# Kernel optimization log

Measured on AMD Instinct MI355X. Metric: run time of the kernel, lower is better.

## Reference

```python
import jax, jax.numpy as jnp
import numpy as np

N, E = 2048, 262144
SDIM, VDIM, EDIM = 256, 64, 32
NUM_ATOM_FEATURES, NUM_BOND_TYPES, NMOL = 16, 5, 64


def setup_inputs() -> dict:
    key = jax.random.key(0)
    ks = jax.random.split(key, 18)
    def lin(k, fan_in, shape):
        return jax.random.uniform(k, shape, jnp.float32, -1.0, 1.0) / np.sqrt(fan_in)
    inp = {
        "s": jax.random.normal(ks[0], (N, SDIM), jnp.float32),
        "v": jax.random.normal(ks[1], (N, 3, VDIM), jnp.float32),
        "p": jax.random.normal(ks[2], (N, 3), jnp.float32),
        "e": jax.random.normal(ks[3], (E, EDIM), jnp.float32),
        "batch": jnp.sort(jax.random.randint(ks[4], (N,), 0, NMOL)),
        "edge_index_global": jax.random.randint(ks[5], (2, E), 0, N),
        # learned params (torch DenseLayer == Linear): W [in,out], b [out]
        "Ws": lin(ks[6], SDIM, (SDIM, SDIM)),   "bs": lin(ks[7], SDIM, (SDIM,)),
        "Wc": lin(ks[8], VDIM, (VDIM, 1)),                                      # coords_lin, no bias
        "Wa": lin(ks[9], SDIM, (SDIM, NUM_ATOM_FEATURES)), "ba": lin(ks[10], SDIM, (NUM_ATOM_FEATURES,)),
        "Wb": lin(ks[11], EDIM, (EDIM, SDIM)),  "bb": lin(ks[12], EDIM, (SDIM,)),
        "W0": lin(ks[13], SDIM + 1, (SDIM + 1, SDIM)), "b0": lin(ks[14], SDIM + 1, (SDIM,)),
        "W1": lin(ks[15], SDIM, (SDIM, NUM_BOND_TYPES)), "b1": lin(ks[16], SDIM, (NUM_BOND_TYPES,)),
    }
    return inp


def reference(s, v, p, e, batch, edge_index_global,
              Ws, bs, Wc, Wa, ba, Wb, bb, W0, b0, W1, b1):
    # shared scalar mapping with SiLU
    s_h = jax.nn.silu(s @ Ws + bs)                              # [N, SDIM]
    coords = (v @ Wc)[..., 0]                                   # [N,3,VDIM]@[VDIM,1] -> [N,3]
    atoms_pred = s_h @ Wa + ba                                  # [N, NUM_ATOM_FEATURES]

    j, i = edge_index_global[0], edge_index_global[1]
    # coords_param == 'data': add positions then remove per-graph mean (scatter_mean)
    coords_pred = p + coords
    sums = jax.ops.segment_sum(coords_pred, batch, num_segments=NMOL)       # [NMOL,3]
    cnts = jax.ops.segment_sum(jnp.ones((N, 1), s.dtype), batch, num_segments=NMOL)
    coords_pred = coords_pred - (sums / jnp.maximum(cnts, 1.0))[batch]

    d = jnp.sum((coords_pred[i] - coords_pred[j]) ** 2, axis=-1, keepdims=True)  # [E,1]

    # dense edge matrix construction + symmetrization (as in the original)
    e_dense = jnp.zeros((N, N, EDIM), e.dtype).at[j, i].set(e)  # [N,N,EDIM]
    e_dense = 0.5 * (e_dense + jnp.swapaxes(e_dense, 0, 1))
    e_sym = e_dense[j, i]                                        # [E,EDIM]

    f = s_h[i] + s_h[j] + (e_sym @ Wb + bb)                      # [E,SDIM]
    edge = jnp.concatenate([f, d], axis=-1)                      # [E,SDIM+1]
    bonds_pred = jax.nn.silu(edge @ W0 + b0) @ W1 + b1           # [E,NUM_BOND_TYPES]
    return coords_pred, atoms_pred, bonds_pred
```

## Files before the change

### kernel.cpp

```cpp
#include <hip/hip_runtime.h>
#include <hip/hip_bf16.h>

typedef __bf16 bf16_8 __attribute__((ext_vector_type(8)));
typedef __bf16 bf16_4 __attribute__((ext_vector_type(4)));
typedef float f32x4 __attribute__((ext_vector_type(4)));

__device__ __forceinline__ float silu_f(float x) {
    return x * __builtin_amdgcn_rcpf(1.0f + __expf(-x));
}

__device__ __forceinline__ unsigned hslot(unsigned cell, unsigned nslots) {
    return (unsigned)(((unsigned long long)(cell * 2654435761u) * nslots) >> 32);
}
__device__ __forceinline__ int map_lookup(unsigned nslots, const int* __restrict__ M,
                                          const unsigned long long* __restrict__ H, unsigned cell) {
    if (nslots == 0) return M[cell] - 1;
    unsigned slot = hslot(cell, nslots);
    for (int pr = 0; pr < 4096; pr++) {
        unsigned long long v = H[slot];
        if (v == 0ull) return -1;
        if ((unsigned)(v >> 32) == cell) return (int)(v & 0xFFFFFFFFu) - 1;
        slot++; if (slot == nslots) slot = 0;
    }
    return -1;
}

__global__ __launch_bounds__(256) void kS(float* __restrict__ out, int n, float val) {
    int i = blockIdx.x * 256 + threadIdx.x;
    if (i < n) out[i] = val;
}

__global__ __launch_bounds__(256, 4) void kP(
    const float* __restrict__ s, const float* __restrict__ Ws, const float* __restrict__ bs,
    const float* __restrict__ W0, const float* __restrict__ Wa, const float* __restrict__ ba,
    const float* __restrict__ v, const float* __restrict__ p,
    const float* __restrict__ Wc, const float* __restrict__ Wb, const float* __restrict__ bb,
    const float* __restrict__ b0, const float* __restrict__ W1,
    const int* __restrict__ batch, const int* __restrict__ ei,
    int N, int E, int gaB, int coordB, int mapB,
    unsigned nslots, int* __restrict__ M, unsigned long long* __restrict__ H,
    __bf16* __restrict__ G, __bf16* __restrict__ wqT, __bf16* __restrict__ w1Tg,
    float* __restrict__ w0L, float* __restrict__ b0p,
    float* __restrict__ cp, float* __restrict__ sums, float* __restrict__ cnts,
    float* __restrict__ outA)
{
    __shared__ __align__(16) char LDSC[37376];
    int b = blockIdx.x, t = threadIdx.x;

    if (b < gaB) {
        __bf16* s_bf  = (__bf16*)LDSC;
        __bf16* sh_bf = (__bf16*)(LDSC + 8448);
        __bf16* wT    = (__bf16*)(LDSC + 16896);
        int wv = t >> 6, lane = t & 63;
        int l16 = lane & 15, q8 = (lane >> 4) * 8, r4b = (lane >> 4) * 4;
        int r0 = b * 16;
        {
            int row = t >> 4, c0 = (t & 15) * 16;
            const float* sp = s + (long long)(r0 + row) * 256 + c0;
            bool ok = (r0 + row) < N;
            f32x4 a0 = ok ? *(const f32x4*)(sp + 0)  : (f32x4){0.f,0.f,0.f,0.f};
            f32x4 a1 = ok ? *(const f32x4*)(sp + 4)  : (f32x4){0.f,0.f,0.f,0.f};
            f32x4 a2 = ok ? *(const f32x4*)(sp + 8)  : (f32x4){0.f,0.f,0.f,0.f};
            f32x4 a3 = ok ? *(const f32x4*)(sp + 12) : (f32x4){0.f,0.f,0.f,0.f};
            bf16_8 p0, p1;
#pragma unroll
            for (int q = 0; q < 4; q++) {
                p0[q] = (__bf16)a0[q]; p0[q + 4] = (__bf16)a1[q];
                p1[q] = (__bf16)a2[q]; p1[q + 4] = (__bf16)a3[q];
            }
            *(bf16_8*)(s_bf + row * 264 + c0) = p0;
            *(bf16_8*)(s_bf + row * 264 + c0 + 8) = p1;
        }
        __syncthreads();
        __bf16* wTw = wT + wv * 2560;
        float ld[32];

        f32x4 acc[4];
#pragma unroll
        for (int ct = 0; ct < 4; ct++) acc[ct] = (f32x4){0.f,0.f,0.f,0.f};
        {
            const float* wp = Ws + wv * 64 + lane;
#pragma unroll
            for (int i = 0; i < 32; i++) ld[i] = wp[i * 256];
#pragma unroll 1
            for (int kk = 0; kk < 8; kk++) {
#pragma unroll
                for (int j = 0; j < 4; j++) {
                    bf16_8 pk;
#pragma unroll
                    for (int q = 0; q < 8; q++) pk[q] = (__bf16)ld[j * 8 + q];
                    *(bf16_8*)(wTw + lane * 40 + j * 8) = pk;
                }
                if (kk < 7) {
                    const float* wpn = wp + (kk + 1) * 32 * 256;
#pragma unroll
                    for (int i = 0; i < 32; i++) ld[i] = wpn[i * 256];
                }
                bf16_8 af = *(const bf16_8*)(s_bf + l16 * 264 + kk * 32 + q8);
#pragma unroll
                for (int ct = 0; ct < 4; ct++) {
                    bf16_8 bfr = *(const bf16_8*)(wTw + (ct * 16 + l16) * 40 + q8);
                    acc[ct] = __builtin_amdgcn_mfma_f32_16x16x32_bf16(af, bfr, acc[ct], 0, 0, 0);
                }
            }
        }
#pragma unroll
        for (int ct = 0; ct < 4; ct++) {
            int col = wv * 64 + ct * 16 + l16;
            float bsv = bs[col];
#pragma unroll
            for (int r = 0; r < 4; r++)
                sh_bf[(r4b + r) * 264 + col] = (__bf16)silu_f(acc[ct][r] + bsv);
        }
        __syncthreads();

        if (wv == 0) {
            f32x4 aa = (f32x4){0.f,0.f,0.f,0.f};
#pragma unroll 1
            for (int ks = 0; ks < 8; ks++) {
                bf16_8 a = *(const bf16_8*)(sh_bf + l16 * 264 + ks * 32 + q8);
                bf16_8 wb;
#pragma unroll
                for (int j = 0; j < 8; j++) wb[j] = (__bf16)Wa[(ks * 32 + q8 + j) * 16 + l16];
                aa = __builtin_amdgcn_mfma_f32_16x16x32_bf16(a, wb, aa, 0, 0, 0);
            }
            float bav = ba[l16];
#pragma unroll
            for (int r = 0; r < 4; r++) {
                int row = r0 + r4b + r;
                if (row < N) outA[row * 16 + l16] = aa[r] + bav;
            }
        }

        f32x4 acc2[4];
#pragma unroll
        for (int ct = 0; ct < 4; ct++) acc2[ct] = (f32x4){0.f,0.f,0.f,0.f};
        {
            const float* wp = W0 + wv * 64 + lane;
#pragma unroll
            for (int i = 0; i < 32; i++) ld[i] = wp[i * 256];
#pragma unroll 1
            for (int kk = 0; kk < 8; kk++) {
#pragma unroll
                for (int j = 0; j < 4; j++) {
                    bf16_8 pk;
#pragma unroll
                    for (int q = 0; q < 8; q++) pk[q] = (__bf16)ld[j * 8 + q];
                    *(bf16_8*)(wTw + lane * 40 + j * 8) = pk;
                }
                if (kk < 7) {
                    const float* wpn = wp + (kk + 1) * 32 * 256;
#pragma unroll
                    for (int i = 0; i < 32; i++) ld[i] = wpn[i * 256];
                }
                bf16_8 af = *(const bf16_8*)(sh_bf + l16 * 264 + kk * 32 + q8);
#pragma unroll
                for (int ct = 0; ct < 4; ct++) {
                    bf16_8 bfr = *(const bf16_8*)(wTw + (ct * 16 + l16) * 40 + q8);
                    acc2[ct] = __builtin_amdgcn_mfma_f32_16x16x32_bf16(af, bfr, acc2[ct], 0, 0, 0);
                }
            }
        }
#pragma unroll
        for (int ct = 0; ct < 4; ct++) {
            int col = wv * 64 + ct * 16 + l16;
#pragma unroll
            for (int r = 0; r < 4; r++) {
                int row = r0 + r4b + r;
                if (row < N) G[(long long)row * 256 + col] = (__bf16)acc2[ct][r];
            }
        }
        return;
    }
    b -= gaB;

    float* sm = (float*)LDSC;
    if (b < 2) {
        int r0 = b * 16;
        for (int i4 = t; i4 < 1024; i4 += 256)
            ((f32x4*)sm)[i4] = ((const f32x4*)(Wb + r0 * 256))[i4];
        __syncthreads();
        float acc[16];
#pragma unroll
        for (int r = 0; r < 16; r++) acc[r] = 0.f;
        for (int m4 = 0; m4 < 64; m4++) {
            float w0v = W0[(m4 * 4 + 0) * 256 + t];
            float w1v = W0[(m4 * 4 + 1) * 256 + t];
            float w2v = W0[(m4 * 4 + 2) * 256 + t];
            float w3v = W0[(m4 * 4 + 3) * 256 + t];
#pragma unroll
            for (int r = 0; r < 16; r++) {
                f32x4 sv = *(const f32x4*)(sm + r * 256 + m4 * 4);
                acc[r] += sv[0] * w0v + sv[1] * w1v + sv[2] * w2v + sv[3] * w3v;
            }
        }
#pragma unroll
        for (int r = 0; r < 16; r++) wqT[t * 32 + r0 + r] = (__bf16)acc[r];
        return;
    }
    b -= 2;
    if (b < 1) {
        sm[t] = bb[t];
        __syncthreads();
        float acc = 0.f;
        for (int m4 = 0; m4 < 64; m4++) {
            f32x4 bv = *(const f32x4*)(sm + m4 * 4);
            acc += bv[0] * W0[(m4 * 4 + 0) * 256 + t] + bv[1] * W0[(m4 * 4 + 1) * 256 + t]
                 + bv[2] * W0[(m4 * 4 + 2) * 256 + t] + bv[3] * W0[(m4 * 4 + 3) * 256 + t];
        }
        b0p[t] = acc + b0[t];
        w0L[t] = W0[256 * 256 + t];
#pragma unroll
        for (int c = 0; c < 16; c++)
            w1Tg[c * 256 + t] = (c < 5) ? (__bf16)W1[t * 5 + c] : (__bf16)0.f;
        return;
    }
    b -= 1;
    if (b < coordB) {
        int n = b * 256 + t;
        if (t < 64) sm[t] = Wc[t];
        __syncthreads();
        if (n < N) {
            int mb = batch[n] & 1023;
#pragma unroll
            for (int ax = 0; ax < 3; ax++) {
                float acc = 0.f;
                for (int d4 = 0; d4 < 16; d4++) {
                    f32x4 vv = *(const f32x4*)(v + (long long)n * 192 + ax * 64 + d4 * 4);
                    f32x4 wv2 = *(const f32x4*)(sm + d4 * 4);
                    acc += vv[0] * wv2[0] + vv[1] * wv2[1] + vv[2] * wv2[2] + vv[3] * wv2[3];
                }
                float val = p[n * 3 + ax] + acc;
                cp[n * 3 + ax] = val;
                atomicAdd(&sums[mb * 3 + ax], val);
            }
            atomicAdd(&cnts[mb], 1.0f);
        }
        return;
    }
    b -= coordB;
    {
        int k = b * 256 + t;
        if (k < E) {
            int jj = ei[k], ii = ei[E + k];
            if ((unsigned)jj >= (unsigned)N) jj = 0;
            if ((unsigned)ii >= (unsigned)N) ii = 0;
            unsigned cell = (unsigned)jj * (unsigned)N + (unsigned)ii;
            if (nslots == 0) {
                atomicMax(&M[cell], k + 1);
            } else {
                unsigned long long mine = ((unsigned long long)cell << 32) | (unsigned)(k + 1);
                unsigned slot = hslot(cell, nslots);
                for (int pr = 0; pr < 4096; pr++) {
                    unsigned long long old = atomicCAS(&H[slot], 0ull, mine);
                    if (old == 0ull) break;
                    if ((unsigned)(old >> 32) == cell) { atomicMax(&H[slot], mine); break; }
                    slot++; if (slot == nslots) slot = 0;
                }
            }
        }
    }
}

__global__ __launch_bounds__(256, 4) void kC(
    const float* __restrict__ e, const int* __restrict__ ei, const int* __restrict__ batch,
    int N, int E, int edgeB, unsigned nslots,
    const int* __restrict__ M, const unsigned long long* __restrict__ H,
    const __bf16* __restrict__ G, const __bf16* __restrict__ wqTg,
    const __bf16* __restrict__ w1Tg,
    const float* __restrict__ w0L, const float* __restrict__ b0p,
    const float* __restrict__ cp, const float* __restrict__ sums, const float* __restrict__ cnts,
    const float* __restrict__ b1,
    float* __restrict__ outC, float* __restrict__ bonds)
{
    if (blockIdx.x >= (unsigned)edgeB) {
        int n = ((int)blockIdx.x - edgeB) * 256 + threadIdx.x;
        if (n < N) {
            int mb = batch[n] & 1023;
            float cnt = fmaxf(cnts[mb], 1.0f);
#pragma unroll
            for (int ax = 0; ax < 3; ax++)
                outC[n * 3 + ax] = cp[n * 3 + ax] - sums[mb * 3 + ax] / cnt;
        }
        return;
    }

    __shared__ __align__(16) __bf16 esym[64 * 40];
    __shared__ __align__(16) __bf16 hbuf[64 * 264];
    __shared__ float sd[64];
    __shared__ int si[64], sj[64], sm1[64], sm2[64];

    int t = threadIdx.x;
    int wv = t >> 6, lane = t & 63;
    int l16 = lane & 15, q8 = (lane >> 4) * 8;
    int e0 = blockIdx.x * 64;

    if (t < 128) {
        int tt = t & 63;
        int k = e0 + tt;
        if (t < 64) {
            if (k >= E) {
                si[tt] = 0; sj[tt] = 0; sm1[tt] = 0; sd[tt] = 0.f;
            } else {
                int jj = ei[k], ii = ei[E + k];
                if ((unsigned)jj >= (unsigned)N) jj = 0;
                if ((unsigned)ii >= (unsigned)N) ii = 0;
                si[tt] = ii; sj[tt] = jj;
                int m1 = map_lookup(nslots, M, H, (unsigned)jj * (unsigned)N + (unsigned)ii);
                sm1[tt] = ((unsigned)m1 < (unsigned)E) ? m1 : 0;
                int bi = batch[ii] & 1023, bj = batch[jj] & 1023;
                float inv_i = __builtin_amdgcn_rcpf(fmaxf(cnts[bi], 1.0f));
                float inv_j = __builtin_amdgcn_rcpf(fmaxf(cnts[bj], 1.0f));
                float dx = (cp[ii * 3 + 0] - sums[bi * 3 + 0] * inv_i) - (cp[jj * 3 + 0] - sums[bj * 3 + 0] * inv_j);
                float dy = (cp[ii * 3 + 1] - sums[bi * 3 + 1] * inv_i) - (cp[jj * 3 + 1] - sums[bj * 3 + 1] * inv_j);
                float dz = (cp[ii * 3 + 2] - sums[bi * 3 + 2] * inv_i) - (cp[jj * 3 + 2] - sums[bj * 3 + 2] * inv_j);
                sd[tt] = dx * dx + dy * dy + dz * dz;
            }
        } else {
            if (k >= E) {
                sm2[tt] = -1;
            } else {
                int jj = ei[k], ii = ei[E + k];
                if ((unsigned)jj >= (unsigned)N) jj = 0;
                if ((unsigned)ii >= (unsigned)N) ii = 0;
                int m2 = map_lookup(nslots, M, H, (unsigned)ii * (unsigned)N + (unsigned)jj);
                sm2[tt] = ((unsigned)m2 < (unsigned)E) ? m2 : -1;
            }
        }
    }
    __syncthreads();

    {
        int er = t >> 2, qg = (t & 3) * 8;
        int m1 = sm1[er], m2 = sm2[er];
        const float* e1p = e + (size_t)m1 * 32 + qg;
        float v1[8], v2[8];
#pragma unroll
        for (int q = 0; q < 8; q++) { v1[q] = e1p[q]; v2[q] = 0.f; }
        if (m2 >= 0) {
            const float* e2p = e + (size_t)m2 * 32 + qg;
#pragma unroll
            for (int q = 0; q < 8; q++) v2[q] = e2p[q];
        }
        bf16_8 es;
#pragma unroll
        for (int q = 0; q < 8; q++) es[q] = (__bf16)(0.5f * (v1[q] + v2[q]));
        *(bf16_8*)(esym + er * 40 + qg) = es;
    }
    {
        int c4 = lane * 4;
        for (int it = 0; it < 16; it++) {
            int er = wv * 16 + it;
            bf16_4 gi = *(const bf16_4*)(G + (size_t)si[er] * 256 + c4);
            bf16_4 gj = *(const bf16_4*)(G + (size_t)sj[er] * 256 + c4);
            bf16_4 o;
#pragma unroll
            for (int q = 0; q < 4; q++) o[q] = (__bf16)((float)gi[q] + (float)gj[q]);
            *(bf16_4*)(hbuf + er * 264 + c4) = o;
        }
    }
    __syncthreads();

    f32x4 acc[4][4];
#pragma unroll
    for (int rt = 0; rt < 4; rt++)
#pragma unroll
        for (int ct = 0; ct < 4; ct++)
            acc[rt][ct] = (f32x4){0.f, 0.f, 0.f, 0.f};
    bf16_8 af[4];
#pragma unroll
    for (int rt = 0; rt < 4; rt++)
        af[rt] = *(const bf16_8*)(esym + (rt * 16 + l16) * 40 + q8);
#pragma unroll
    for (int ct = 0; ct < 4; ct++) {
        int c = (wv * 4 + ct) * 16 + l16;
        bf16_8 bfr = *(const bf16_8*)(wqTg + c * 32 + q8);
#pragma unroll
        for (int rt = 0; rt < 4; rt++)
            acc[rt][ct] = __builtin_amdgcn_mfma_f32_16x16x32_bf16(af[rt], bfr, acc[rt][ct], 0, 0, 0);
    }
    int r4base = (lane >> 4) * 4;
    f32x4 sdv[4];
#pragma unroll
    for (int rt = 0; rt < 4; rt++)
        sdv[rt] = *(const f32x4*)(sd + rt * 16 + r4base);
#pragma unroll
    for (int ct = 0; ct < 4; ct++) {
        int col = (wv * 4 + ct) * 16 + l16;
        float w0c = w0L[col], b0c = b0p[col];
#pragma unroll
        for (int rt = 0; rt < 4; rt++) {
#pragma unroll
            for (int r4 = 0; r4 < 4; r4++) {
                int row = rt * 16 + r4base + r4;
                int off = row * 264 + col;
                float x = acc[rt][ct][r4] + b0c + sdv[rt][r4] * w0c + (float)hbuf[off];
                hbuf[off] = (__bf16)silu_f(x);
            }
        }
    }
    __syncthreads();

    f32x4 acc3 = {0.f, 0.f, 0.f, 0.f};
#pragma unroll
    for (int ks = 0; ks < 8; ks++) {
        bf16_8 a = *(const bf16_8*)(hbuf + (wv * 16 + l16) * 264 + ks * 32 + q8);
        bf16_8 b2 = *(const bf16_8*)(w1Tg + l16 * 256 + ks * 32 + q8);
        acc3 = __builtin_amdgcn_mfma_f32_16x16x32_bf16(a, b2, acc3, 0, 0, 0);
    }
    if (l16 < 5) {
        float bv = b1[l16];
#pragma unroll
        for (int r4 = 0; r4 < 4; r4++) {
            int row = wv * 16 + r4base + r4;
            if (e0 + row < E)
                bonds[(size_t)(e0 + row) * 5 + l16] = acc3[r4] + bv;
        }
    }
}

extern "C" void kernel_launch(void* const* d_in, const int* in_sizes, int n_in,
                              void* d_out, int out_size, void* d_ws, size_t ws_size,
                              hipStream_t stream)
{
    const float* s  = (const float*)d_in[0];
    const float* v  = (const float*)d_in[1];
    const float* p  = (const float*)d_in[2];
    const float* e  = (const float*)d_in[3];
    const int* batch = (const int*)d_in[4];
    const int* ei    = (const int*)d_in[5];
    const float* Ws = (const float*)d_in[6];
    const float* bs = (const float*)d_in[7];
    const float* Wc = (const float*)d_in[8];
    const float* Wa = (const float*)d_in[9];
    const float* ba = (const float*)d_in[10];
    const float* Wb = (const float*)d_in[11];
    const float* bb = (const float*)d_in[12];
    const float* W0 = (const float*)d_in[13];
    const float* b0 = (const float*)d_in[14];
    const float* W1 = (const float*)d_in[15];
    const float* b1 = (const float*)d_in[16];

    float* out = (float*)d_out;
    int sentN = out_size < 8192 ? out_size : 8192;

    int N = in_sizes[0] / 256;
    long long E = in_sizes[5] / 2;
    int code = 0;
    if (in_sizes[6] != 65536) code |= 1;
    if (in_sizes[8] != 64) code |= 2;
    if (in_sizes[11] != 32 * 256) code |= 4;
    if (in_sizes[9] != 16 * 256) code |= 8;
    if (in_sizes[15] != 5 * 256) code |= 16;
    if (in_sizes[13] != 257 * 256) code |= 32;
    if (N < 1 || in_sizes[0] != N * 256) code |= 64;
    if (in_sizes[1] != (long long)N * 192) code |= 128;
    if (in_sizes[2] != N * 3) code |= 256;
    if (in_sizes[3] != E * 32) code |= 512;
    if (in_sizes[4] != N) code |= 1024;
    if ((long long)out_size != 19LL * N + 5LL * E) code |= 2048;
    if (code) {
        kS<<<(sentN + 255) / 256, 256, 0, stream>>>(out, sentN, 3000.0f + 64.0f * (float)code);
        return;
    }
    int Ei = (int)E;

    auto align256 = [](size_t x) { return (x + 255) & ~(size_t)255; };
    size_t G_b  = align256((size_t)N * 512);
    size_t cp_b = align256((size_t)N * 12);
    size_t misc = G_b + 16384 + 8192 + 1024 + 1024 + cp_b + 12288 + 4096 + 256;
    size_t denseB = (size_t)N * (size_t)N * 4;
    unsigned nslots; size_t mapBytes;
    if (ws_size >= denseB + misc) {
        nslots = 0; mapBytes = denseB;
    } else {
        size_t avail = (ws_size > misc) ? (ws_size - misc) / 8 : 0;
        size_t want = (size_t)Ei * 2;
        size_t ns = avail < want ? avail : want;
        if (ns < (size_t)Ei + (size_t)Ei / 8) {
            unsigned mb = (unsigned)(ws_size >> 20); if (mb > 120) mb = 120;
            kS<<<(sentN + 255) / 256, 256, 0, stream>>>(out, sentN, 1000.0f + 8.0f * (float)mb);
            return;
        }
        nslots = (unsigned)ns; mapBytes = ns * 8;
    }

    char* ws = (char*)d_ws;
    int* M = (int*)ws;
    unsigned long long* H = (unsigned long long*)ws;
    size_t off = align256(mapBytes);
    __bf16* G    = (__bf16*)(ws + off); off += G_b;
    __bf16* wqT  = (__bf16*)(ws + off); off += 16384;
    __bf16* w1Tg = (__bf16*)(ws + off); off += 8192;
    float* w0L  = (float*)(ws + off);  off += 1024;
    float* b0p  = (float*)(ws + off);  off += 1024;
    float* cp   = (float*)(ws + off);  off += cp_b;
    float* sums = (float*)(ws + off);  off += 12288;
    float* cnts = (float*)(ws + off);  off += 4096;

    float* outC = out;
    float* outA = outC + 3 * N;
    float* outB = outC + 19 * N;

    (void)hipMemsetAsync(ws, 0x00, mapBytes, stream);
    (void)hipMemsetAsync(sums, 0x00, 12288 + 4096, stream);

    int mapB = (Ei + 255) / 256;
    int coordB = (N + 255) / 256;
    int gaB = (N + 15) / 16;
    kP<<<gaB + 3 + coordB + mapB, 256, 0, stream>>>(
        s, Ws, bs, W0, Wa, ba, v, p, Wc, Wb, bb, b0, W1, batch, ei,
        N, Ei, gaB, coordB, mapB, nslots, M, H,
        G, wqT, w1Tg, w0L, b0p, cp, sums, cnts, outA);
    int edgeB = (Ei + 63) / 64;
    kC<<<edgeB + coordB, 256, 0, stream>>>(
        e, ei, batch, N, Ei, edgeB, nslots, M, H, G, wqT, w1Tg,
        w0L, b0p, cp, sums, cnts, b1, outC, outB);
}
```

Before: 196.1 us.

## Split weight prep into separate kernel, pre-transpose weights, restructure edge MLP

Weight conversion to transposed bf16 (Ws, W0, Wa) moves into a new prep kernel kW. The node GEMM kernel kP is split four ways across column quarters and reads the pre-transposed weights directly from global memory instead of restaging them through LDS. The two hipMemsetAsync calls are replaced by one custom zero kernel. In the edge kernel, the G gather and the bias/SiLU epilogue are fused into registers per edge, so the hbuf staging pass and one block barrier are removed. In exchange there is one more kernel launch and the first node-level GEMM is recomputed four times per row block.

```diff
diff --git a/kernel.cpp b/kernel.cpp
--- a/kernel.cpp
+++ b/kernel.cpp
@@ -30,151 +30,30 @@
     if (i < n) out[i] = val;
 }
 
-__global__ __launch_bounds__(256, 4) void kP(
-    const float* __restrict__ s, const float* __restrict__ Ws, const float* __restrict__ bs,
-    const float* __restrict__ W0, const float* __restrict__ Wa, const float* __restrict__ ba,
+__global__ __launch_bounds__(256) void kZ(f32x4* __restrict__ a, size_t na16,
+                                          f32x4* __restrict__ b, size_t nb16) {
+    size_t i = (size_t)blockIdx.x * 256 + threadIdx.x;
+    size_t stride = (size_t)gridDim.x * 256;
+    f32x4 z = {0.f, 0.f, 0.f, 0.f};
+    for (size_t k = i; k < na16; k += stride) a[k] = z;
+    for (size_t k = i; k < nb16; k += stride) b[k] = z;
+}
+
+__global__ __launch_bounds__(256) void kW(
     const float* __restrict__ v, const float* __restrict__ p,
-    const float* __restrict__ Wc, const float* __restrict__ Wb, const float* __restrict__ bb,
-    const float* __restrict__ b0, const float* __restrict__ W1,
     const int* __restrict__ batch, const int* __restrict__ ei,
-    int N, int E, int gaB, int coordB, int mapB,
+    const float* __restrict__ Wc, const float* __restrict__ Ws, const float* __restrict__ Wa,
+    const float* __restrict__ Wb, const float* __restrict__ bb,
+    const float* __restrict__ W0, const float* __restrict__ b0, const float* __restrict__ W1,
+    int N, int E, int coordB, int mapB,
     unsigned nslots, int* __restrict__ M, unsigned long long* __restrict__ H,
-    __bf16* __restrict__ G, __bf16* __restrict__ wqT, __bf16* __restrict__ w1Tg,
+    __bf16* __restrict__ wqT, __bf16* __restrict__ w1Tg,
+    __bf16* __restrict__ WsT, __bf16* __restrict__ W0T, __bf16* __restrict__ WaT,
     float* __restrict__ w0L, float* __restrict__ b0p,
-    float* __restrict__ cp, float* __restrict__ sums, float* __restrict__ cnts,
-    float* __restrict__ outA)
+    float* __restrict__ cp, float* __restrict__ sums, float* __restrict__ cnts)
 {
-    __shared__ __align__(16) char LDSC[37376];
+    __shared__ float sm[16 * 256];
     int b = blockIdx.x, t = threadIdx.x;
-
-    if (b < gaB) {
-        __bf16* s_bf  = (__bf16*)LDSC;
-        __bf16* sh_bf = (__bf16*)(LDSC + 8448);
-        __bf16* wT    = (__bf16*)(LDSC + 16896);
-        int wv = t >> 6, lane = t & 63;
-        int l16 = lane & 15, q8 = (lane >> 4) * 8, r4b = (lane >> 4) * 4;
-        int r0 = b * 16;
-        {
-            int row = t >> 4, c0 = (t & 15) * 16;
-            const float* sp = s + (long long)(r0 + row) * 256 + c0;
-            bool ok = (r0 + row) < N;
-            f32x4 a0 = ok ? *(const f32x4*)(sp + 0)  : (f32x4){0.f,0.f,0.f,0.f};
-            f32x4 a1 = ok ? *(const f32x4*)(sp + 4)  : (f32x4){0.f,0.f,0.f,0.f};
-            f32x4 a2 = ok ? *(const f32x4*)(sp + 8)  : (f32x4){0.f,0.f,0.f,0.f};
-            f32x4 a3 = ok ? *(const f32x4*)(sp + 12) : (f32x4){0.f,0.f,0.f,0.f};
-            bf16_8 p0, p1;
-#pragma unroll
-            for (int q = 0; q < 4; q++) {
-                p0[q] = (__bf16)a0[q]; p0[q + 4] = (__bf16)a1[q];
-                p1[q] = (__bf16)a2[q]; p1[q + 4] = (__bf16)a3[q];
-            }
-            *(bf16_8*)(s_bf + row * 264 + c0) = p0;
-            *(bf16_8*)(s_bf + row * 264 + c0 + 8) = p1;
-        }
-        __syncthreads();
-        __bf16* wTw = wT + wv * 2560;
-        float ld[32];
-
-        f32x4 acc[4];
-#pragma unroll
-        for (int ct = 0; ct < 4; ct++) acc[ct] = (f32x4){0.f,0.f,0.f,0.f};
-        {
-            const float* wp = Ws + wv * 64 + lane;
-#pragma unroll
-            for (int i = 0; i < 32; i++) ld[i] = wp[i * 256];
-#pragma unroll 1
-            for (int kk = 0; kk < 8; kk++) {
-#pragma unroll
-                for (int j = 0; j < 4; j++) {
-                    bf16_8 pk;
-#pragma unroll
-                    for (int q = 0; q < 8; q++) pk[q] = (__bf16)ld[j * 8 + q];
-                    *(bf16_8*)(wTw + lane * 40 + j * 8) = pk;
-                }
-                if (kk < 7) {
-                    const float* wpn = wp + (kk + 1) * 32 * 256;
-#pragma unroll
-                    for (int i = 0; i < 32; i++) ld[i] = wpn[i * 256];
-                }
-                bf16_8 af = *(const bf16_8*)(s_bf + l16 * 264 + kk * 32 + q8);
-#pragma unroll
-                for (int ct = 0; ct < 4; ct++) {
-                    bf16_8 bfr = *(const bf16_8*)(wTw + (ct * 16 + l16) * 40 + q8);
-                    acc[ct] = __builtin_amdgcn_mfma_f32_16x16x32_bf16(af, bfr, acc[ct], 0, 0, 0);
-                }
-            }
-        }
-#pragma unroll
-        for (int ct = 0; ct < 4; ct++) {
-            int col = wv * 64 + ct * 16 + l16;
-            float bsv = bs[col];
-#pragma unroll
-            for (int r = 0; r < 4; r++)
-                sh_bf[(r4b + r) * 264 + col] = (__bf16)silu_f(acc[ct][r] + bsv);
-        }
-        __syncthreads();
-
-        if (wv == 0) {
-            f32x4 aa = (f32x4){0.f,0.f,0.f,0.f};
-#pragma unroll 1
-            for (int ks = 0; ks < 8; ks++) {
-                bf16_8 a = *(const bf16_8*)(sh_bf + l16 * 264 + ks * 32 + q8);
-                bf16_8 wb;
-#pragma unroll
-                for (int j = 0; j < 8; j++) wb[j] = (__bf16)Wa[(ks * 32 + q8 + j) * 16 + l16];
-                aa = __builtin_amdgcn_mfma_f32_16x16x32_bf16(a, wb, aa, 0, 0, 0);
-            }
-            float bav = ba[l16];
-#pragma unroll
-            for (int r = 0; r < 4; r++) {
-                int row = r0 + r4b + r;
-                if (row < N) outA[row * 16 + l16] = aa[r] + bav;
-            }
-        }
-
-        f32x4 acc2[4];
-#pragma unroll
-        for (int ct = 0; ct < 4; ct++) acc2[ct] = (f32x4){0.f,0.f,0.f,0.f};
-        {
-            const float* wp = W0 + wv * 64 + lane;
-#pragma unroll
-            for (int i = 0; i < 32; i++) ld[i] = wp[i * 256];
-#pragma unroll 1
-            for (int kk = 0; kk < 8; kk++) {
-#pragma unroll
-                for (int j = 0; j < 4; j++) {
-                    bf16_8 pk;
-#pragma unroll
-                    for (int q = 0; q < 8; q++) pk[q] = (__bf16)ld[j * 8 + q];
-                    *(bf16_8*)(wTw + lane * 40 + j * 8) = pk;
-                }
-                if (kk < 7) {
-                    const float* wpn = wp + (kk + 1) * 32 * 256;
-#pragma unroll
-                    for (int i = 0; i < 32; i++) ld[i] = wpn[i * 256];
-                }
-                bf16_8 af = *(const bf16_8*)(sh_bf + l16 * 264 + kk * 32 + q8);
-#pragma unroll
-                for (int ct = 0; ct < 4; ct++) {
-                    bf16_8 bfr = *(const bf16_8*)(wTw + (ct * 16 + l16) * 40 + q8);
-                    acc2[ct] = __builtin_amdgcn_mfma_f32_16x16x32_bf16(af, bfr, acc2[ct], 0, 0, 0);
-                }
-            }
-        }
-#pragma unroll
-        for (int ct = 0; ct < 4; ct++) {
-            int col = wv * 64 + ct * 16 + l16;
-#pragma unroll
-            for (int r = 0; r < 4; r++) {
-                int row = r0 + r4b + r;
-                if (row < N) G[(long long)row * 256 + col] = (__bf16)acc2[ct][r];
-            }
-        }
-        return;
-    }
-    b -= gaB;
-
-    float* sm = (float*)LDSC;
     if (b < 2) {
         int r0 = b * 16;
         for (int i4 = t; i4 < 1024; i4 += 256)
@@ -213,6 +92,30 @@
 #pragma unroll
         for (int c = 0; c < 16; c++)
             w1Tg[c * 256 + t] = (c < 5) ? (__bf16)W1[t * 5 + c] : (__bf16)0.f;
+        return;
+    }
+    b -= 1;
+    if (b < 4) {
+        for (int idx = t; idx < 64 * 256; idx += 256) {
+            int kl = idx >> 8, c = idx & 255;
+            WsT[c * 256 + b * 64 + kl] = (__bf16)Ws[(b * 64 + kl) * 256 + c];
+        }
+        return;
+    }
+    b -= 4;
+    if (b < 4) {
+        for (int idx = t; idx < 64 * 256; idx += 256) {
+            int kl = idx >> 8, c = idx & 255;
+            W0T[c * 256 + b * 64 + kl] = (__bf16)W0[(b * 64 + kl) * 256 + c];
+        }
+        return;
+    }
+    b -= 4;
+    if (b < 1) {
+        for (int idx = t; idx < 4096; idx += 256) {
+            int k = idx >> 4, c = idx & 15;
+            WaT[c * 256 + k] = (__bf16)Wa[k * 16 + c];
+        }
         return;
     }
     b -= 1;
@@ -262,6 +165,91 @@
     }
 }
 
+__global__ __launch_bounds__(256, 4) void kP(
+    const float* __restrict__ s, const float* __restrict__ bs, const float* __restrict__ ba,
+    const __bf16* __restrict__ WsT, const __bf16* __restrict__ W0T, const __bf16* __restrict__ WaT,
+    int N, __bf16* __restrict__ G, float* __restrict__ outA)
+{
+    __shared__ __align__(16) __bf16 s_bf[16 * 264];
+    __shared__ __align__(16) __bf16 sh_bf[16 * 264];
+    int b = blockIdx.x, t = threadIdx.x;
+    int rb = b >> 2, cq = b & 3;
+    int r0 = rb * 16;
+    int wv = t >> 6, lane = t & 63;
+    int l16 = lane & 15, q = lane >> 4, q8 = q * 8;
+
+    {
+        int row = t >> 4, c0 = (t & 15) * 16;
+        const float* sp = s + (long long)(r0 + row) * 256 + c0;
+        bool ok = (r0 + row) < N;
+        f32x4 a0 = ok ? *(const f32x4*)(sp + 0)  : (f32x4){0.f,0.f,0.f,0.f};
+        f32x4 a1 = ok ? *(const f32x4*)(sp + 4)  : (f32x4){0.f,0.f,0.f,0.f};
+        f32x4 a2 = ok ? *(const f32x4*)(sp + 8)  : (f32x4){0.f,0.f,0.f,0.f};
+        f32x4 a3 = ok ? *(const f32x4*)(sp + 12) : (f32x4){0.f,0.f,0.f,0.f};
+        bf16_8 p0, p1;
+#pragma unroll
+        for (int qq = 0; qq < 4; qq++) {
+            p0[qq] = (__bf16)a0[qq]; p0[qq + 4] = (__bf16)a1[qq];
+            p1[qq] = (__bf16)a2[qq]; p1[qq + 4] = (__bf16)a3[qq];
+        }
+        *(bf16_8*)(s_bf + row * 264 + c0) = p0;
+        *(bf16_8*)(s_bf + row * 264 + c0 + 8) = p1;
+    }
+    __syncthreads();
+
+    f32x4 acc[4];
+#pragma unroll
+    for (int ct = 0; ct < 4; ct++) acc[ct] = (f32x4){0.f,0.f,0.f,0.f};
+#pragma unroll
+    for (int kk = 0; kk < 8; kk++) {
+        bf16_8 af = *(const bf16_8*)(s_bf + l16 * 264 + kk * 32 + q8);
+#pragma unroll
+        for (int ct = 0; ct < 4; ct++) {
+            bf16_8 bw = *(const bf16_8*)(WsT + (size_t)(wv * 64 + ct * 16 + l16) * 256 + kk * 32 + q8);
+            acc[ct] = __builtin_amdgcn_mfma_f32_16x16x32_bf16(af, bw, acc[ct], 0, 0, 0);
+        }
+    }
+#pragma unroll
+    for (int ct = 0; ct < 4; ct++) {
+        int col = wv * 64 + ct * 16 + l16;
+        float bsv = bs[col];
+#pragma unroll
+        for (int r = 0; r < 4; r++)
+            sh_bf[(q * 4 + r) * 264 + col] = (__bf16)silu_f(acc[ct][r] + bsv);
+    }
+    __syncthreads();
+
+    f32x4 a2c = (f32x4){0.f,0.f,0.f,0.f};
+    int gcol = cq * 64 + wv * 16 + l16;
+#pragma unroll
+    for (int kk = 0; kk < 8; kk++) {
+        bf16_8 af = *(const bf16_8*)(sh_bf + l16 * 264 + kk * 32 + q8);
+        bf16_8 bw = *(const bf16_8*)(W0T + (size_t)gcol * 256 + kk * 32 + q8);
+        a2c = __builtin_amdgcn_mfma_f32_16x16x32_bf16(af, bw, a2c, 0, 0, 0);
+    }
+#pragma unroll
+    for (int r = 0; r < 4; r++) {
+        int row = r0 + q * 4 + r;
+        if (row < N) G[(long long)row * 256 + gcol] = (__bf16)a2c[r];
+    }
+
+    if (cq == 0 && wv == 0) {
+        f32x4 aa = (f32x4){0.f,0.f,0.f,0.f};
+#pragma unroll
+        for (int ks = 0; ks < 8; ks++) {
+            bf16_8 af = *(const bf16_8*)(sh_bf + l16 * 264 + ks * 32 + q8);
+            bf16_8 bw = *(const bf16_8*)(WaT + (size_t)l16 * 256 + ks * 32 + q8);
+            aa = __builtin_amdgcn_mfma_f32_16x16x32_bf16(af, bw, aa, 0, 0, 0);
+        }
+        float bav = ba[l16];
+#pragma unroll
+        for (int r = 0; r < 4; r++) {
+            int row = r0 + q * 4 + r;
+            if (row < N) outA[row * 16 + l16] = aa[r] + bav;
+        }
+    }
+}
+
 __global__ __launch_bounds__(256, 4) void kC(
     const float* __restrict__ e, const int* __restrict__ ei, const int* __restrict__ batch,
     int N, int E, int edgeB, unsigned nslots,
@@ -292,7 +280,7 @@
 
     int t = threadIdx.x;
     int wv = t >> 6, lane = t & 63;
-    int l16 = lane & 15, q8 = (lane >> 4) * 8;
+    int l16 = lane & 15, q = lane >> 4, q8 = q * 8;
     int e0 = blockIdx.x * 64;
 
     if (t < 128) {
@@ -336,70 +324,48 @@
         const float* e1p = e + (size_t)m1 * 32 + qg;
         float v1[8], v2[8];
 #pragma unroll
-        for (int q = 0; q < 8; q++) { v1[q] = e1p[q]; v2[q] = 0.f; }
+        for (int qq = 0; qq < 8; qq++) { v1[qq] = e1p[qq]; v2[qq] = 0.f; }
         if (m2 >= 0) {
             const float* e2p = e + (size_t)m2 * 32 + qg;
 #pragma unroll
-            for (int q = 0; q < 8; q++) v2[q] = e2p[q];
+            for (int qq = 0; qq < 8; qq++) v2[qq] = e2p[qq];
         }
         bf16_8 es;
 #pragma unroll
-        for (int q = 0; q < 8; q++) es[q] = (__bf16)(0.5f * (v1[q] + v2[q]));
+        for (int qq = 0; qq < 8; qq++) es[qq] = (__bf16)(0.5f * (v1[qq] + v2[qq]));
         *(bf16_8*)(esym + er * 40 + qg) = es;
     }
-    {
-        int c4 = lane * 4;
-        for (int it = 0; it < 16; it++) {
-            int er = wv * 16 + it;
-            bf16_4 gi = *(const bf16_4*)(G + (size_t)si[er] * 256 + c4);
-            bf16_4 gj = *(const bf16_4*)(G + (size_t)sj[er] * 256 + c4);
-            bf16_4 o;
-#pragma unroll
-            for (int q = 0; q < 4; q++) o[q] = (__bf16)((float)gi[q] + (float)gj[q]);
-            *(bf16_4*)(hbuf + er * 264 + c4) = o;
-        }
-    }
-    __syncthreads();
-
-    f32x4 acc[4][4];
-#pragma unroll
-    for (int rt = 0; rt < 4; rt++)
-#pragma unroll
-        for (int ct = 0; ct < 4; ct++)
-            acc[rt][ct] = (f32x4){0.f, 0.f, 0.f, 0.f};
-    bf16_8 af[4];
-#pragma unroll
-    for (int rt = 0; rt < 4; rt++)
-        af[rt] = *(const bf16_8*)(esym + (rt * 16 + l16) * 40 + q8);
-#pragma unroll
-    for (int ct = 0; ct < 4; ct++) {
-        int c = (wv * 4 + ct) * 16 + l16;
-        bf16_8 bfr = *(const bf16_8*)(wqTg + c * 32 + q8);
-#pragma unroll
-        for (int rt = 0; rt < 4; rt++)
-            acc[rt][ct] = __builtin_amdgcn_mfma_f32_16x16x32_bf16(af[rt], bfr, acc[rt][ct], 0, 0, 0);
-    }
-    int r4base = (lane >> 4) * 4;
-    f32x4 sdv[4];
-#pragma unroll
-    for (int rt = 0; rt < 4; rt++)
-        sdv[rt] = *(const f32x4*)(sd + rt * 16 + r4base);
-#pragma unroll
-    for (int ct = 0; ct < 4; ct++) {
-        int col = (wv * 4 + ct) * 16 + l16;
-        float w0c = w0L[col], b0c = b0p[col];
-#pragma unroll
-        for (int rt = 0; rt < 4; rt++) {
-#pragma unroll
-            for (int r4 = 0; r4 < 4; r4++) {
-                int row = rt * 16 + r4base + r4;
-                int off = row * 264 + col;
-                float x = acc[rt][ct][r4] + b0c + sdv[rt][r4] * w0c + (float)hbuf[off];
-                hbuf[off] = (__bf16)silu_f(x);
-            }
-        }
-    }
-    __syncthreads();
+
+    int ew = wv * 16 + l16;
+    int ii = si[ew], jj = sj[ew];
+    float d = sd[ew];
+    const __bf16* Gi = G + (size_t)ii * 256;
+    const __bf16* Gj = G + (size_t)jj * 256;
+    bf16_8 be = *(const bf16_8*)(esym + ew * 40 + q8);
+
+    f32x4 acc[16];
+#pragma unroll
+    for (int rt = 0; rt < 16; rt++) acc[rt] = (f32x4){0.f, 0.f, 0.f, 0.f};
+#pragma unroll
+    for (int rt = 0; rt < 16; rt++) {
+        bf16_8 aw = *(const bf16_8*)(wqTg + (rt * 16 + l16) * 32 + q8);
+        acc[rt] = __builtin_amdgcn_mfma_f32_16x16x32_bf16(aw, be, acc[rt], 0, 0, 0);
+    }
+#pragma unroll
+    for (int rt = 0; rt < 16; rt++) {
+        int oc = rt * 16 + q * 4;
+        bf16_4 gi = *(const bf16_4*)(Gi + oc);
+        bf16_4 gj = *(const bf16_4*)(Gj + oc);
+        f32x4 b0v = *(const f32x4*)(b0p + oc);
+        f32x4 w0v = *(const f32x4*)(w0L + oc);
+        bf16_4 o;
+#pragma unroll
+        for (int r = 0; r < 4; r++) {
+            float x = acc[rt][r] + b0v[r] + d * w0v[r] + (float)gi[r] + (float)gj[r];
+            o[r] = (__bf16)silu_f(x);
+        }
+        *(bf16_4*)(hbuf + ew * 264 + oc) = o;
+    }
 
     f32x4 acc3 = {0.f, 0.f, 0.f, 0.f};
 #pragma unroll
@@ -411,10 +377,10 @@
     if (l16 < 5) {
         float bv = b1[l16];
 #pragma unroll
-        for (int r4 = 0; r4 < 4; r4++) {
-            int row = wv * 16 + r4base + r4;
+        for (int r = 0; r < 4; r++) {
+            int row = wv * 16 + q * 4 + r;
             if (e0 + row < E)
-                bonds[(size_t)(e0 + row) * 5 + l16] = acc3[r4] + bv;
+                bonds[(size_t)(e0 + row) * 5 + l16] = acc3[r] + bv;
         }
     }
 }
@@ -468,7 +434,8 @@
     auto align256 = [](size_t x) { return (x + 255) & ~(size_t)255; };
     size_t G_b  = align256((size_t)N * 512);
     size_t cp_b = align256((size_t)N * 12);
-    size_t misc = G_b + 16384 + 8192 + 1024 + 1024 + cp_b + 12288 + 4096 + 256;
+    size_t misc = G_b + 16384 + 8192 + 131072 + 131072 + 8192
+                + 1024 + 1024 + cp_b + 12288 + 4096 + 256;
     size_t denseB = (size_t)N * (size_t)N * 4;
     unsigned nslots; size_t mapBytes;
     if (ws_size >= denseB + misc) {
@@ -488,10 +455,14 @@
     char* ws = (char*)d_ws;
     int* M = (int*)ws;
     unsigned long long* H = (unsigned long long*)ws;
-    size_t off = align256(mapBytes);
+    size_t mapZ = align256(mapBytes);
+    size_t off = mapZ;
     __bf16* G    = (__bf16*)(ws + off); off += G_b;
     __bf16* wqT  = (__bf16*)(ws + off); off += 16384;
     __bf16* w1Tg = (__bf16*)(ws + off); off += 8192;
+    __bf16* WsT  = (__bf16*)(ws + off); off += 131072;
+    __bf16* W0T  = (__bf16*)(ws + off); off += 131072;
+    __bf16* WaT  = (__bf16*)(ws + off); off += 8192;
     float* w0L  = (float*)(ws + off);  off += 1024;
     float* b0p  = (float*)(ws + off);  off += 1024;
     float* cp   = (float*)(ws + off);  off += cp_b;
@@ -502,16 +473,17 @@
     float* outA = outC + 3 * N;
     float* outB = outC + 19 * N;
 
-    (void)hipMemsetAsync(ws, 0x00, mapBytes, stream);
-    (void)hipMemsetAsync(sums, 0x00, 12288 + 4096, stream);
+    kZ<<<2048, 256, 0, stream>>>((f32x4*)ws, mapZ >> 4, (f32x4*)sums, 1024);
 
     int mapB = (Ei + 255) / 256;
     int coordB = (N + 255) / 256;
-    int gaB = (N + 15) / 16;
-    kP<<<gaB + 3 + coordB + mapB, 256, 0, stream>>>(
-        s, Ws, bs, W0, Wa, ba, v, p, Wc, Wb, bb, b0, W1, batch, ei,
-        N, Ei, gaB, coordB, mapB, nslots, M, H,
-        G, wqT, w1Tg, w0L, b0p, cp, sums, cnts, outA);
+    kW<<<2 + 1 + 4 + 4 + 1 + coordB + mapB, 256, 0, stream>>>(
+        v, p, batch, ei, Wc, Ws, Wa, Wb, bb, W0, b0, W1,
+        N, Ei, coordB, mapB, nslots, M, H,
+        wqT, w1Tg, WsT, W0T, WaT, w0L, b0p, cp, sums, cnts);
+    int rbB = (N + 15) / 16;
+    kP<<<rbB * 4, 256, 0, stream>>>(
+        s, bs, ba, WsT, W0T, WaT, N, G, outA);
     int edgeB = (Ei + 63) / 64;
     kC<<<edgeB + coordB, 256, 0, stream>>>(
         e, ei, batch, N, Ei, edgeB, nslots, M, H, G, wqT, w1Tg,
```

Result: slower. 272.4 us (+38.9%).
